# Kernel optimization log

Hardware: AMD Instinct MI355X
Metric: run time of the kernel (lower is better)

The kernel has to match this reference:

```python
import jax, jax.numpy as jnp
import numpy as np


def conv2d_reflect(x, w, b, stride):
    # 3x3 conv, padding=1, padding_mode='reflect'
    x = jnp.pad(x, ((0, 0), (0, 0), (1, 1), (1, 1)), mode='reflect')
    y = jax.lax.conv_general_dilated(x, w, (stride, stride), 'VALID',
                                     dimension_numbers=('NCHW', 'OIHW', 'NCHW'))
    return y + b[None, :, None, None]


def avg_pool(x, k):
    B, C, H, W = x.shape
    return x.reshape(B, C, H // k, k, W // k, k).mean(axis=(3, 5))


def _interp_axis(x, size_out, axis):
    # 1D linear interpolation with align_corners=True semantics
    size_in = x.shape[axis]
    pos = jnp.linspace(0.0, size_in - 1.0, size_out)
    i0 = jnp.clip(jnp.floor(pos).astype(jnp.int32), 0, size_in - 2)
    frac = (pos - i0.astype(x.dtype))
    shape = [1] * x.ndim
    shape[axis] = size_out
    frac = frac.reshape(shape)
    a = jnp.take(x, i0, axis=axis)
    b = jnp.take(x, i0 + 1, axis=axis)
    return a + frac * (b - a)


def resize_bilinear_ac(x, oh, ow):
    return _interp_axis(_interp_axis(x, oh, 2), ow, 3)


def _forward(img, conv1_w, conv1_b, conv2_w, conv2_b, conv3_w, conv3_b,
             conv4_w, conv4_b, lin1_w, lin1_b, lin2_w, lin2_b, luts):
    B, C, H, W = img.shape
    silu = jax.nn.silu
    # --- feature branch on fixed 256x256 resize ---
    x = resize_bilinear_ac(img, 256, 256)
    c1 = silu(conv2d_reflect(x, conv1_w, conv1_b, 2))    # [B,32,128,128]
    c2 = silu(conv2d_reflect(c1, conv2_w, conv2_b, 2))   # [B,64,64,64]
    c3 = silu(conv2d_reflect(c2, conv3_w, conv3_b, 2))   # [B,128,32,32]
    c4 = silu(conv2d_reflect(c3, conv4_w, conv4_b, 2))   # [B,256,16,16]
    feat = jnp.concatenate([avg_pool(c1, 16), avg_pool(c2, 8),
                            avg_pool(c3, 4), avg_pool(c4, 2)], axis=1)  # [B,480,8,8]
    h1 = silu(conv2d_reflect(feat, lin1_w, lin1_b, 1))   # [B,128,8,8]
    wl = jax.lax.conv_general_dilated(h1, lin2_w, (1, 1), 'VALID',
                                      dimension_numbers=('NCHW', 'OIHW', 'NCHW'))
    wl = jax.nn.sigmoid(wl + lin2_b[None, :, None, None])  # [B,27,8,8]
    weights = resize_bilinear_ac(wl, H, W)               # [B, C*K, H, W]
    # --- adaptive 1D LUT transform (per-pixel interpolated gather) ---
    Cl, K, N = luts.shape
    pos = jnp.clip(img, 0.0, 1.0) * (N - 1)
    i0 = jnp.clip(jnp.floor(pos).astype(jnp.int32), 0, N - 2)  # [B,C,H,W]
    frac = pos - i0.astype(pos.dtype)
    cidx = jnp.arange(Cl)[None, :, None, None, None]
    kidx = jnp.arange(K)[None, None, :, None, None]
    iexp = i0[:, :, None, :, :]
    v0 = luts[cidx, kidx, iexp]          # [B,C,K,H,W]
    v1 = luts[cidx, kidx, iexp + 1]
    val = v0 + frac[:, :, None, :, :] * (v1 - v0)
    wts = weights.reshape(B, Cl, K, H, W)
    return jnp.einsum('bckhw,bckhw->bchw', wts, val)


def setup_inputs() -> dict:
    key = jax.random.key(0)
    ks = jax.random.split(key, 10)
    s = 0.05
    return {
        'img': jax.random.uniform(ks[0], (2, 3, 1024, 1024), dtype=jnp.float32),
        'conv1_w': jax.random.normal(ks[1], (32, 3, 3, 3), dtype=jnp.float32) * s,
        'conv1_b': jnp.zeros((32,), jnp.float32),
        'conv2_w': jax.random.normal(ks[2], (64, 32, 3, 3), dtype=jnp.float32) * s,
        'conv2_b': jnp.zeros((64,), jnp.float32),
        'conv3_w': jax.random.normal(ks[3], (128, 64, 3, 3), dtype=jnp.float32) * s,
        'conv3_b': jnp.zeros((128,), jnp.float32),
        'conv4_w': jax.random.normal(ks[4], (256, 128, 3, 3), dtype=jnp.float32) * s,
        'conv4_b': jnp.zeros((256,), jnp.float32),
        'lin1_w': jax.random.normal(ks[5], (128, 480, 3, 3), dtype=jnp.float32) * s,
        'lin1_b': jnp.zeros((128,), jnp.float32),
        'lin2_w': jax.random.normal(ks[6], (27, 128, 1, 1), dtype=jnp.float32) * s,
        'lin2_b': jnp.zeros((27,), jnp.float32),
        'luts': jax.random.normal(ks[7], (3, 9, 256), dtype=jnp.float32),
    }


def reference(img, conv1_w, conv1_b, conv2_w, conv2_b, conv3_w, conv3_b,
              conv4_w, conv4_b, lin1_w, lin1_b, lin2_w, lin2_b, luts):
    out = _forward(img, conv1_w, conv1_b, conv2_w, conv2_b, conv3_w, conv3_b,
                   conv4_w, conv4_b, lin1_w, lin1_b, lin2_w, lin2_b, luts)
    return jnp.clip(out, 0.0, 1.0)
```

## Files before the change

kernel.cpp:

```cpp
#include <hip/hip_runtime.h>

#define DI __device__ __forceinline__

DI float silu_f(float x) { return x / (1.f + __expf(-x)); }
DI float sigmoid_f(float x) { return 1.f / (1.f + __expf(-x)); }
DI int reflect_i(int i, int n) { if (i < 0) i = -i; if (i >= n) i = 2 * n - 2 - i; return i; }

__global__ __launch_bounds__(256) void k_resize(const float* __restrict__ img,
                                                float* __restrict__ x) {
    __shared__ float r0s[1024], r1s[1024];
    const int oy = blockIdx.x & 255;
    const int bc = blockIdx.x >> 8;
    float py = oy * (1023.f / 255.f);
    int iy0 = (int)py; if (iy0 > 1022) iy0 = 1022;
    float fy = py - (float)iy0;
    const float* p0 = img + ((size_t)bc * 1024 + iy0) * 1024;
    ((float4*)r0s)[threadIdx.x] = ((const float4*)p0)[threadIdx.x];
    ((float4*)r1s)[threadIdx.x] = ((const float4*)(p0 + 1024))[threadIdx.x];
    __syncthreads();
    const int ox = threadIdx.x;
    float px = ox * (1023.f / 255.f);
    int ix0 = (int)px; if (ix0 > 1022) ix0 = 1022;
    float fx = px - (float)ix0;
    float a00 = r0s[ix0], a01 = r0s[ix0 + 1];
    float a10 = r1s[ix0], a11 = r1s[ix0 + 1];
    float r0v = a00 + fy * (a10 - a00);
    float r1v = a01 + fy * (a11 - a01);
    x[((size_t)bc * 256 + oy) * 256 + ox] = r0v + fx * (r1v - r0v);
}

template<int CIN, int HIN, int WIN, int COUT, int OCW>
__global__ __launch_bounds__(256) void k_conv_woc(const float* __restrict__ in,
                                                  const float* __restrict__ w,
                                                  const float* __restrict__ bias,
                                                  float* __restrict__ out) {
    constexpr int HOUT = HIN / 2, WOUT = WIN / 2;
    constexpr int NB_PX = 2 * HOUT * WOUT / 64;
    constexpr int NOC = 4 * OCW;
    constexpr int PL = HIN * WIN;

    __shared__ float sw[NOC * CIN * 12];
    const int tid = threadIdx.x;
    const int ocu = blockIdx.x / NB_PX;
    const int bpx = blockIdx.x % NB_PX;
    {
        const float* src = w + (size_t)(ocu * NOC) * CIN * 9;
        for (int i = tid; i < NOC * CIN * 9; i += 256)
            sw[(i / 9) * 12 + (i % 9)] = src[i];
    }
    __syncthreads();

    const int wave = tid >> 6, lane = tid & 63;
    const int pxu = bpx * 64 + lane;
    const int ox = pxu % WOUT;
    const int oy = (pxu / WOUT) % HOUT;
    const int bb = pxu / (WOUT * HOUT);

    int off[9];
#pragma unroll
    for (int ky = 0; ky < 3; ++ky) {
        int ry = reflect_i(2 * oy + ky - 1, HIN) * WIN;
#pragma unroll
        for (int kx = 0; kx < 3; ++kx)
            off[ky * 3 + kx] = ry + reflect_i(2 * ox + kx - 1, WIN);
    }

    float acc[OCW];
#pragma unroll
    for (int o = 0; o < OCW; ++o) acc[o] = 0.f;
    const float* swb = sw + (size_t)(wave * OCW) * CIN * 12;
    const float* base = in + (size_t)bb * CIN * PL;

    if constexpr (CIN % 2 == 0) {
        for (int ic = 0; ic < CIN; ic += 2) {
            float t0[9], t1[9];
#pragma unroll
            for (int j = 0; j < 9; ++j) t0[j] = base[off[j]];
#pragma unroll
            for (int j = 0; j < 9; ++j) t1[j] = base[PL + off[j]];
#pragma unroll
            for (int o = 0; o < OCW; ++o) {
                const float* wp = swb + ((size_t)o * CIN + ic) * 12;
#pragma unroll
                for (int j = 0; j < 9; ++j) acc[o] = fmaf(t0[j], wp[j], acc[o]);
#pragma unroll
                for (int j = 0; j < 9; ++j) acc[o] = fmaf(t1[j], wp[12 + j], acc[o]);
            }
            base += 2 * PL;
        }
    } else {
#pragma unroll
        for (int ic = 0; ic < CIN; ++ic) {
            float t0[9];
#pragma unroll
            for (int j = 0; j < 9; ++j) t0[j] = base[off[j]];
#pragma unroll
            for (int o = 0; o < OCW; ++o) {
                const float* wp = swb + ((size_t)o * CIN + ic) * 12;
#pragma unroll
                for (int j = 0; j < 9; ++j) acc[o] = fmaf(t0[j], wp[j], acc[o]);
            }
            base += PL;
        }
    }

#pragma unroll
    for (int o = 0; o < OCW; ++o) {
        const int oc = ocu * NOC + wave * OCW + o;
        out[(((size_t)bb * COUT + oc) * HOUT + oy) * WOUT + ox] =
            silu_f(acc[o] + bias[oc]);
    }
}

template<int CIN, int HIN, int WIN, int COUT, int OC_PER>
__global__ __launch_bounds__(256) void k_conv_w4(const float* __restrict__ in,
                                                 const float* __restrict__ w,
                                                 const float* __restrict__ bias,
                                                 float* __restrict__ out) {
    constexpr int HOUT = HIN / 2, WOUT = WIN / 2;
    constexpr int NB_PX = 2 * HOUT * WOUT / 64;
    constexpr int ICC = CIN / 4;
    constexpr int PL = HIN * WIN;
    static_assert(ICC % 2 == 0, "ICC even");

    __shared__ float sw[OC_PER * CIN * 12];
    __shared__ float sred[4][OC_PER][64];
    const int tid = threadIdx.x;
    const int ocu = blockIdx.x / NB_PX;
    const int bpx = blockIdx.x % NB_PX;
    {
        const float* src = w + (size_t)(ocu * OC_PER) * CIN * 9;
        for (int i = tid; i < OC_PER * CIN * 9; i += 256)
            sw[(i / 9) * 12 + (i % 9)] = src[i];
    }
    __syncthreads();

    const int kc = tid >> 6;
    const int lane = tid & 63;
    const int pxu = bpx * 64 + lane;
    const int ox = pxu % WOUT;
    const int oy = (pxu / WOUT) % HOUT;
    const int bb = pxu / (WOUT * HOUT);

    int off[9];
#pragma unroll
    for (int ky = 0; ky < 3; ++ky) {
        int ry = reflect_i(2 * oy + ky - 1, HIN) * WIN;
#pragma unroll
        for (int kx = 0; kx < 3; ++kx)
            off[ky * 3 + kx] = ry + reflect_i(2 * ox + kx - 1, WIN);
    }

    float acc[OC_PER];
#pragma unroll
    for (int o = 0; o < OC_PER; ++o) acc[o] = 0.f;
    const float* base = in + ((size_t)bb * CIN + kc * ICC) * PL;

    for (int icl = 0; icl < ICC; icl += 2) {
        float t0[9], t1[9];
#pragma unroll
        for (int j = 0; j < 9; ++j) t0[j] = base[off[j]];
#pragma unroll
        for (int j = 0; j < 9; ++j) t1[j] = base[PL + off[j]];
#pragma unroll
        for (int o = 0; o < OC_PER; ++o) {
            const float* wp = sw + ((size_t)o * CIN + kc * ICC + icl) * 12;
#pragma unroll
            for (int j = 0; j < 9; ++j) acc[o] = fmaf(t0[j], wp[j], acc[o]);
#pragma unroll
            for (int j = 0; j < 9; ++j) acc[o] = fmaf(t1[j], wp[12 + j], acc[o]);
        }
        base += 2 * PL;
    }

#pragma unroll
    for (int o = 0; o < OC_PER; ++o) sred[kc][o][lane] = acc[o];
    __syncthreads();
    if (kc < OC_PER) {
        const int o = kc;
        const int oc = ocu * OC_PER + o;
        float s = sred[0][o][lane] + sred[1][o][lane] + sred[2][o][lane] + sred[3][o][lane];
        out[(((size_t)bb * COUT + oc) * HOUT + oy) * WOUT + ox] = silu_f(s + bias[oc]);
    }
}

__global__ __launch_bounds__(256) void k_pool(const float* __restrict__ c1,
                                              const float* __restrict__ c2,
                                              const float* __restrict__ c3,
                                              const float* __restrict__ c4,
                                              float* __restrict__ feat) {
    const int tid = threadIdx.x;
    const int W = blockIdx.x * 4 + (tid >> 6);
    const int lane = tid & 63;
    if (W < 512) {
        int bb = W >> 8, rem = W & 255;
        int c = rem >> 3, y = rem & 7;
        const float* p = c1 + ((size_t)bb * 32 + c) * 128 * 128 + (y * 16) * 128 + lane * 2;
        float s = 0.f;
#pragma unroll
        for (int r = 0; r < 16; ++r) {
            float2 v = *(const float2*)(p + r * 128);
            s += v.x + v.y;
        }
        s += __shfl_xor(s, 1, 64);
        s += __shfl_xor(s, 2, 64);
        s += __shfl_xor(s, 4, 64);
        if ((lane & 7) == 0)
            feat[((size_t)bb * 480 + c) * 64 + y * 8 + (lane >> 3)] = s * (1.f / 256.f);
    } else if (W < 1536) {
        int V = W - 512;
        int bb = V >> 9, rem = V & 511;
        int c = rem >> 3, y = rem & 7;
        const float* p = c2 + ((size_t)bb * 64 + c) * 64 * 64 + (y * 8) * 64 + lane;
        float s = 0.f;
#pragma unroll
        for (int r = 0; r < 8; ++r) s += p[r * 64];
        s += __shfl_xor(s, 1, 64);
        s += __shfl_xor(s, 2, 64);
        s += __shfl_xor(s, 4, 64);
        if ((lane & 7) == 0)
            feat[((size_t)bb * 480 + 32 + c) * 64 + y * 8 + (lane >> 3)] = s * (1.f / 64.f);
    } else if (W < 1792) {
        int T = (W - 1536) * 64 + lane;
        int bb = T >> 13, rem = T & 8191;
        int c = rem >> 6, y = (rem >> 3) & 7, x = rem & 7;
        const float* p = c3 + ((size_t)bb * 128 + c) * 32 * 32 + (y * 4) * 32 + x * 4;
        float s = 0.f;
#pragma unroll
        for (int r = 0; r < 4; ++r) {
            float4 v = *(const float4*)(p + r * 32);
            s += v.x + v.y + v.z + v.w;
        }
        feat[((size_t)bb * 480 + 96 + c) * 64 + y * 8 + x] = s * (1.f / 16.f);
    } else {
        int T = (W - 1792) * 64 + lane;
        int bb = T >> 14, rem = T & 16383;
        int c = rem >> 6, y = (rem >> 3) & 7, x = rem & 7;
        const float* p = c4 + ((size_t)bb * 256 + c) * 16 * 16 + (y * 2) * 16 + x * 2;
        float2 v0 = *(const float2*)p;
        float2 v1 = *(const float2*)(p + 16);
        feat[((size_t)bb * 480 + 224 + c) * 64 + y * 8 + x] = (v0.x + v0.y + v1.x + v1.y) * 0.25f;
    }
}

__global__ __launch_bounds__(512) void k_lin1(const float* __restrict__ feat,
                                              const float* __restrict__ w,
                                              const float* __restrict__ bias,
                                              float* __restrict__ h1) {
    __shared__ float sw[480 * 9];
    __shared__ float sred[8][64];
    const int tid = threadIdx.x;
    const int bb = blockIdx.x >> 7;
    const int oc = blockIdx.x & 127;
    {
        const float* src = w + (size_t)oc * 480 * 9;
        for (int i = tid; i < 480 * 9; i += 512) sw[i] = src[i];
    }
    const int wave = tid >> 6;
    const int lane = tid & 63;
    const int py = lane >> 3, px = lane & 7;
    int srcl[9];
#pragma unroll
    for (int ky = 0; ky < 3; ++ky)
#pragma unroll
        for (int kx = 0; kx < 3; ++kx)
            srcl[ky * 3 + kx] = reflect_i(py + ky - 1, 8) * 8 + reflect_i(px + kx - 1, 8);
    __syncthreads();

    const float* fp = feat + (size_t)bb * 480 * 64;
    float acc = 0.f;
    for (int ic = wave * 60; ic < wave * 60 + 60; ++ic) {
        float v = fp[ic * 64 + lane];
        const float* wp = sw + ic * 9;
#pragma unroll
        for (int j = 0; j < 9; ++j)
            acc = fmaf(__shfl(v, srcl[j], 64), wp[j], acc);
    }
    sred[wave][lane] = acc;
    __syncthreads();
    if (wave == 0) {
        float s = 0.f;
#pragma unroll
        for (int wv = 0; wv < 8; ++wv) s += sred[wv][lane];
        h1[((size_t)bb * 128 + oc) * 64 + lane] = silu_f(s + bias[oc]);
    }
}

__global__ __launch_bounds__(256) void k_apply(const float* __restrict__ img,
                                               const float* __restrict__ h1,
                                               const float* __restrict__ l2w,
                                               const float* __restrict__ l2b,
                                               const float* __restrict__ luts,
                                               float* __restrict__ out) {
    __shared__ float2 slut2[9 * 256];
    __shared__ float swl[9 * 64];
    __shared__ float su4[4 * 72];
    const int tid = threadIdx.x;
    const int bc = blockIdx.y;
    const int bb = bc / 3, c = bc % 3;
    const int wave = tid >> 6, pix = tid & 63;

    for (int i = tid; i < 9 * 256; i += 256) {
        int k = i >> 8, j = i & 255;
        const float* lp = luts + (size_t)(c * 9 + k) * 256;
        float v0 = lp[j];
        float v1 = lp[j < 255 ? j + 1 : 255];
        slut2[i] = make_float2(v0, v1);
    }
    {
        const float* hp = h1 + (size_t)bb * 128 * 64;
        for (int o = wave; o < 9; o += 4) {
            const float* wp = l2w + (size_t)(c * 9 + o) * 128;
            float s = l2b[c * 9 + o];
            for (int ic = 0; ic < 128; ++ic) s = fmaf(hp[ic * 64 + pix], wp[ic], s);
            swl[o * 64 + pix] = sigmoid_f(s);
        }
    }
    __syncthreads();
    for (int i = tid; i < 288; i += 256) {
        int rr = i / 72, rem = i % 72;
        int k = rem >> 3, xx = rem & 7;
        int h = blockIdx.x * 4 + rr;
        float py = h * (7.f / 1023.f);
        int iy0 = (int)py; if (iy0 > 6) iy0 = 6;
        float fy = py - (float)iy0;
        float a = swl[k * 64 + iy0 * 8 + xx];
        float b = swl[k * 64 + iy0 * 8 + 8 + xx];
        su4[i] = fmaf(fy, b - a, a);
    }
    __syncthreads();

    const int x0 = tid * 4;
    float fx[4]; int sel[4]; int cbase;
    {
        float p0 = x0 * (7.f / 1023.f);
        int ib = (int)p0; if (ib > 6) ib = 6;
        cbase = ib;
#pragma unroll
        for (int p = 0; p < 4; ++p) {
            float pxf = (x0 + p) * (7.f / 1023.f);
            int i = (int)pxf; if (i > 6) i = 6;
            sel[p] = i - cbase;
            fx[p] = pxf - (float)i;
        }
    }
    const size_t plane = ((size_t)bb * 3 + c) * 1024;
    const int h0 = blockIdx.x * 4;

    float4 v = ((const float4*)(img + (plane + h0) * 1024))[tid];
    for (int rr = 0; rr < 4; ++rr) {
        float4 vn = v;
        if (rr < 3) vn = ((const float4*)(img + (plane + h0 + rr + 1) * 1024))[tid];
        float xin[4] = {v.x, v.y, v.z, v.w};
        int i0[4]; float fr[4]; float acc[4] = {0.f, 0.f, 0.f, 0.f};
#pragma unroll
        for (int p = 0; p < 4; ++p) {
            float pv = fminf(fmaxf(xin[p], 0.f), 1.f) * 255.f;
            int i = (int)pv; if (i > 254) i = 254;
            i0[p] = i; fr[p] = pv - (float)i;
        }
        const float* srow = su4 + rr * 72;
#pragma unroll
        for (int k = 0; k < 9; ++k) {
            float s0 = srow[k * 8 + cbase];
            float s1 = srow[k * 8 + cbase + 1];
            float s2 = (cbase < 6) ? srow[k * 8 + cbase + 2] : s1;
            const float2* lrow = slut2 + k * 256;
#pragma unroll
            for (int p = 0; p < 4; ++p) {
                float a = sel[p] ? s1 : s0;
                float b = sel[p] ? s2 : s1;
                float wt = fmaf(fx[p], b - a, a);
                float2 l = lrow[i0[p]];
                acc[p] = fmaf(wt, fmaf(fr[p], l.y - l.x, l.x), acc[p]);
            }
        }
        float4 o4 = make_float4(fminf(fmaxf(acc[0], 0.f), 1.f),
                                fminf(fmaxf(acc[1], 0.f), 1.f),
                                fminf(fmaxf(acc[2], 0.f), 1.f),
                                fminf(fmaxf(acc[3], 0.f), 1.f));
        ((float4*)(out + (plane + h0 + rr) * 1024))[tid] = o4;
        v = vn;
    }
}

extern "C" void kernel_launch(void* const* d_in, const int* in_sizes, int n_in,
                              void* d_out, int out_size, void* d_ws, size_t ws_size,
                              hipStream_t stream) {
    const float* img     = (const float*)d_in[0];
    const float* conv1_w = (const float*)d_in[1];
    const float* conv1_b = (const float*)d_in[2];
    const float* conv2_w = (const float*)d_in[3];
    const float* conv2_b = (const float*)d_in[4];
    const float* conv3_w = (const float*)d_in[5];
    const float* conv3_b = (const float*)d_in[6];
    const float* conv4_w = (const float*)d_in[7];
    const float* conv4_b = (const float*)d_in[8];
    const float* lin1_w  = (const float*)d_in[9];
    const float* lin1_b  = (const float*)d_in[10];
    const float* lin2_w  = (const float*)d_in[11];
    const float* lin2_b  = (const float*)d_in[12];
    const float* luts    = (const float*)d_in[13];
    float* out = (float*)d_out;

    float* ws = (float*)d_ws;
    float* x_rs = ws;            ws += 2 * 3 * 256 * 256;
    float* c1   = ws;            ws += 2 * 32 * 128 * 128;
    float* c2   = ws;            ws += 2 * 64 * 64 * 64;
    float* c3   = ws;            ws += 2 * 128 * 32 * 32;
    float* c4   = ws;            ws += 2 * 256 * 16 * 16;
    float* feat = ws;            ws += 2 * 480 * 8 * 8;
    float* h1   = ws;            ws += 2 * 128 * 8 * 8;

    const int B = 256;
    k_resize<<<6 * 256, B, 0, stream>>>(img, x_rs);
    k_conv_woc<3, 256, 256, 32, 2><<<2048, B, 0, stream>>>(x_rs, conv1_w, conv1_b, c1);
    k_conv_woc<32, 128, 128, 64, 1><<<2048, B, 0, stream>>>(c1, conv2_w, conv2_b, c2);
    k_conv_w4<64, 64, 64, 128, 2><<<2048, B, 0, stream>>>(c2, conv3_w, conv3_b, c3);
    k_conv_w4<128, 32, 32, 256, 2><<<1024, B, 0, stream>>>(c3, conv4_w, conv4_b, c4);
    k_pool<<<576, B, 0, stream>>>(c1, c2, c3, c4, feat);
    k_lin1<<<256, 512, 0, stream>>>(feat, lin1_w, lin1_b, h1);
    dim3 agrid(256, 6);
    k_apply<<<agrid, B, 0, stream>>>(img, h1, lin2_w, lin2_b, luts, out);
}
```

Measured before the change: 278.5 us.

## Replace strided conv kernels with LDS-tiled row-block convolution

Replaces the two per-pixel global-gather conv kernels with one templated kernel. Each block stages a band of reflected input rows for a chunk of input channels in shared memory. Each thread then computes several output channels (and up to two pixels) from that band, writing float2 where possible. This aims to cut redundant global/L2 gathers and raise arithmetic reuse per loaded value, but it shrinks the grids to 128–256 blocks, which may leave many CUs idle.

```diff
diff --git a/kernel.cpp b/kernel.cpp
--- a/kernel.cpp
+++ b/kernel.cpp
@@ -29,158 +29,105 @@
     x[((size_t)bc * 256 + oy) * 256 + ox] = r0v + fx * (r1v - r0v);
 }
 
-template<int CIN, int HIN, int WIN, int COUT, int OCW>
-__global__ __launch_bounds__(256) void k_conv_woc(const float* __restrict__ in,
+template<int CIN, int HIN, int WIN, int COUT, int ROWS, int OCB, int ICB, int PXPT>
+__global__ __launch_bounds__(256) void k_conv_lds(const float* __restrict__ in,
                                                   const float* __restrict__ w,
                                                   const float* __restrict__ bias,
                                                   float* __restrict__ out) {
     constexpr int HOUT = HIN / 2, WOUT = WIN / 2;
-    constexpr int NB_PX = 2 * HOUT * WOUT / 64;
-    constexpr int NOC = 4 * OCW;
-    constexpr int PL = HIN * WIN;
-
-    __shared__ float sw[NOC * CIN * 12];
+    constexpr int NR = 2 * ROWS + 1;
+    constexpr int WINP = WIN + 4;
+    constexpr int NRG = HOUT / ROWS;
+    constexpr int NOCG = COUT / OCB;
+    constexpr int XT = WOUT / PXPT;
+    static_assert(ROWS * XT == 256, "block = 256 threads");
+    static_assert(CIN % ICB == 0, "ICB divides CIN");
+
+    __shared__ float sIn[ICB * NR * WINP];
+    __shared__ float sw[OCB * CIN * 12];
+
     const int tid = threadIdx.x;
-    const int ocu = blockIdx.x / NB_PX;
-    const int bpx = blockIdx.x % NB_PX;
+    const int ocg = blockIdx.x % NOCG;
+    const int rg  = (blockIdx.x / NOCG) % NRG;
+    const int bb  = blockIdx.x / (NOCG * NRG);
+
     {
-        const float* src = w + (size_t)(ocu * NOC) * CIN * 9;
-        for (int i = tid; i < NOC * CIN * 9; i += 256)
+        const float* src = w + (size_t)(ocg * OCB) * CIN * 9;
+        for (int i = tid; i < OCB * CIN * 9; i += 256)
             sw[(i / 9) * 12 + (i % 9)] = src[i];
     }
-    __syncthreads();
-
-    const int wave = tid >> 6, lane = tid & 63;
-    const int pxu = bpx * 64 + lane;
-    const int ox = pxu % WOUT;
-    const int oy = (pxu / WOUT) % HOUT;
-    const int bb = pxu / (WOUT * HOUT);
-
-    int off[9];
-#pragma unroll
-    for (int ky = 0; ky < 3; ++ky) {
-        int ry = reflect_i(2 * oy + ky - 1, HIN) * WIN;
+
+    const int xt = tid % XT;
+    const int r  = tid / XT;
+    const int x0 = xt * PXPT;
+    const int oy0 = rg * ROWS;
+    const int row0 = 2 * oy0 - 1;
+
+    int xs[3 * PXPT];
+#pragma unroll
+    for (int p = 0; p < PXPT; ++p)
 #pragma unroll
         for (int kx = 0; kx < 3; ++kx)
-            off[ky * 3 + kx] = ry + reflect_i(2 * ox + kx - 1, WIN);
-    }
-
-    float acc[OCW];
-#pragma unroll
-    for (int o = 0; o < OCW; ++o) acc[o] = 0.f;
-    const float* swb = sw + (size_t)(wave * OCW) * CIN * 12;
-    const float* base = in + (size_t)bb * CIN * PL;
-
-    if constexpr (CIN % 2 == 0) {
-        for (int ic = 0; ic < CIN; ic += 2) {
-            float t0[9], t1[9];
-#pragma unroll
-            for (int j = 0; j < 9; ++j) t0[j] = base[off[j]];
-#pragma unroll
-            for (int j = 0; j < 9; ++j) t1[j] = base[PL + off[j]];
-#pragma unroll
-            for (int o = 0; o < OCW; ++o) {
-                const float* wp = swb + ((size_t)o * CIN + ic) * 12;
-#pragma unroll
-                for (int j = 0; j < 9; ++j) acc[o] = fmaf(t0[j], wp[j], acc[o]);
-#pragma unroll
-                for (int j = 0; j < 9; ++j) acc[o] = fmaf(t1[j], wp[12 + j], acc[o]);
+            xs[kx * PXPT + p] = reflect_i(2 * (x0 + p) + kx - 1, WIN);
+
+    float acc[OCB][PXPT];
+#pragma unroll
+    for (int o = 0; o < OCB; ++o)
+#pragma unroll
+        for (int p = 0; p < PXPT; ++p) acc[o][p] = 0.f;
+
+    constexpr int W4 = WIN / 4;
+    constexpr int UN = ICB * NR * W4;
+
+    for (int ic0 = 0; ic0 < CIN; ic0 += ICB) {
+        __syncthreads();
+        for (int u = tid; u < UN; u += 256) {
+            const int p   = u / (NR * W4);
+            const int rem = u % (NR * W4);
+            const int lr  = rem / W4;
+            const int c4  = rem % W4;
+            const int grow = reflect_i(row0 + lr, HIN);
+            const float4 v = *(const float4*)(in +
+                ((size_t)(bb * CIN + ic0 + p) * HIN + grow) * WIN + 4 * c4);
+            *(float4*)&sIn[(p * NR + lr) * WINP + 4 * c4] = v;
+        }
+        __syncthreads();
+
+        for (int ic = 0; ic < ICB; ++ic) {
+            const float* ibase = sIn + (ic * NR + 2 * r) * WINP;
+            float t[3][3 * PXPT];
+#pragma unroll
+            for (int ky = 0; ky < 3; ++ky) {
+                const float* rp = ibase + ky * WINP;
+#pragma unroll
+                for (int j = 0; j < 3 * PXPT; ++j) t[ky][j] = rp[xs[j]];
             }
-            base += 2 * PL;
-        }
-    } else {
-#pragma unroll
-        for (int ic = 0; ic < CIN; ++ic) {
-            float t0[9];
-#pragma unroll
-            for (int j = 0; j < 9; ++j) t0[j] = base[off[j]];
-#pragma unroll
-            for (int o = 0; o < OCW; ++o) {
-                const float* wp = swb + ((size_t)o * CIN + ic) * 12;
-#pragma unroll
-                for (int j = 0; j < 9; ++j) acc[o] = fmaf(t0[j], wp[j], acc[o]);
+#pragma unroll
+            for (int o = 0; o < OCB; ++o) {
+                const float* wp = sw + ((size_t)o * CIN + ic0 + ic) * 12;
+#pragma unroll
+                for (int ky = 0; ky < 3; ++ky)
+#pragma unroll
+                    for (int kx = 0; kx < 3; ++kx)
+#pragma unroll
+                        for (int p = 0; p < PXPT; ++p)
+                            acc[o][p] = fmaf(t[ky][kx * PXPT + p], wp[ky * 3 + kx], acc[o][p]);
             }
-            base += PL;
-        }
-    }
-
-#pragma unroll
-    for (int o = 0; o < OCW; ++o) {
-        const int oc = ocu * NOC + wave * OCW + o;
-        out[(((size_t)bb * COUT + oc) * HOUT + oy) * WOUT + ox] =
-            silu_f(acc[o] + bias[oc]);
-    }
-}
-
-template<int CIN, int HIN, int WIN, int COUT, int OC_PER>
-__global__ __launch_bounds__(256) void k_conv_w4(const float* __restrict__ in,
-                                                 const float* __restrict__ w,
-                                                 const float* __restrict__ bias,
-                                                 float* __restrict__ out) {
-    constexpr int HOUT = HIN / 2, WOUT = WIN / 2;
-    constexpr int NB_PX = 2 * HOUT * WOUT / 64;
-    constexpr int ICC = CIN / 4;
-    constexpr int PL = HIN * WIN;
-    static_assert(ICC % 2 == 0, "ICC even");
-
-    __shared__ float sw[OC_PER * CIN * 12];
-    __shared__ float sred[4][OC_PER][64];
-    const int tid = threadIdx.x;
-    const int ocu = blockIdx.x / NB_PX;
-    const int bpx = blockIdx.x % NB_PX;
-    {
-        const float* src = w + (size_t)(ocu * OC_PER) * CIN * 9;
-        for (int i = tid; i < OC_PER * CIN * 9; i += 256)
-            sw[(i / 9) * 12 + (i % 9)] = src[i];
-    }
-    __syncthreads();
-
-    const int kc = tid >> 6;
-    const int lane = tid & 63;
-    const int pxu = bpx * 64 + lane;
-    const int ox = pxu % WOUT;
-    const int oy = (pxu / WOUT) % HOUT;
-    const int bb = pxu / (WOUT * HOUT);
-
-    int off[9];
-#pragma unroll
-    for (int ky = 0; ky < 3; ++ky) {
-        int ry = reflect_i(2 * oy + ky - 1, HIN) * WIN;
-#pragma unroll
-        for (int kx = 0; kx < 3; ++kx)
-            off[ky * 3 + kx] = ry + reflect_i(2 * ox + kx - 1, WIN);
-    }
-
-    float acc[OC_PER];
-#pragma unroll
-    for (int o = 0; o < OC_PER; ++o) acc[o] = 0.f;
-    const float* base = in + ((size_t)bb * CIN + kc * ICC) * PL;
-
-    for (int icl = 0; icl < ICC; icl += 2) {
-        float t0[9], t1[9];
-#pragma unroll
-        for (int j = 0; j < 9; ++j) t0[j] = base[off[j]];
-#pragma unroll
-        for (int j = 0; j < 9; ++j) t1[j] = base[PL + off[j]];
-#pragma unroll
-        for (int o = 0; o < OC_PER; ++o) {
-            const float* wp = sw + ((size_t)o * CIN + kc * ICC + icl) * 12;
-#pragma unroll
-            for (int j = 0; j < 9; ++j) acc[o] = fmaf(t0[j], wp[j], acc[o]);
-#pragma unroll
-            for (int j = 0; j < 9; ++j) acc[o] = fmaf(t1[j], wp[12 + j], acc[o]);
-        }
-        base += 2 * PL;
-    }
-
-#pragma unroll
-    for (int o = 0; o < OC_PER; ++o) sred[kc][o][lane] = acc[o];
-    __syncthreads();
-    if (kc < OC_PER) {
-        const int o = kc;
-        const int oc = ocu * OC_PER + o;
-        float s = sred[0][o][lane] + sred[1][o][lane] + sred[2][o][lane] + sred[3][o][lane];
-        out[(((size_t)bb * COUT + oc) * HOUT + oy) * WOUT + ox] = silu_f(s + bias[oc]);
+        }
+    }
+
+#pragma unroll
+    for (int o = 0; o < OCB; ++o) {
+        const int oc = ocg * OCB + o;
+        const float bv = bias[oc];
+        float* op = out + ((size_t)(bb * COUT + oc) * HOUT + oy0 + r) * WOUT + x0;
+        if (PXPT == 2) {
+            float2 v = make_float2(silu_f(acc[o][0] + bv), silu_f(acc[o][1] + bv));
+            *(float2*)op = v;
+        } else {
+#pragma unroll
+            for (int p = 0; p < PXPT; ++p) op[p] = silu_f(acc[o][p] + bv);
+        }
     }
 }
 
@@ -414,10 +361,10 @@
 
     const int B = 256;
     k_resize<<<6 * 256, B, 0, stream>>>(img, x_rs);
-    k_conv_woc<3, 256, 256, 32, 2><<<2048, B, 0, stream>>>(x_rs, conv1_w, conv1_b, c1);
-    k_conv_woc<32, 128, 128, 64, 1><<<2048, B, 0, stream>>>(c1, conv2_w, conv2_b, c2);
-    k_conv_w4<64, 64, 64, 128, 2><<<2048, B, 0, stream>>>(c2, conv3_w, conv3_b, c3);
-    k_conv_w4<128, 32, 32, 256, 2><<<1024, B, 0, stream>>>(c3, conv4_w, conv4_b, c4);
+    k_conv_lds<3, 256, 256, 32, 4, 16, 3, 2><<<128, B, 0, stream>>>(x_rs, conv1_w, conv1_b, c1);
+    k_conv_lds<32, 128, 128, 64, 4, 8, 8, 1><<<256, B, 0, stream>>>(c1, conv2_w, conv2_b, c2);
+    k_conv_lds<64, 64, 64, 128, 8, 8, 8, 1><<<128, B, 0, stream>>>(c2, conv3_w, conv3_b, c3);
+    k_conv_lds<128, 32, 32, 256, 16, 4, 8, 1><<<128, B, 0, stream>>>(c3, conv4_w, conv4_b, c4);
     k_pool<<<576, B, 0, stream>>>(c1, c2, c3, c4, feat);
     k_lin1<<<256, 512, 0, stream>>>(feat, lin1_w, lin1_b, h1);
     dim3 agrid(256, 6);
```

Result: slower. 330.9 us (+18.8%).
